# Optimization experiments

Hardware: AMD Instinct MI355X
Metric: run time of the kernel (lower is better)

## Reference

```python
import jax, jax.numpy as jnp
import numpy as np

N_LEVELS = 16
N_FEAT = 2
LOG2_HASHMAP = 19
HASHMAP_SIZE = 1 << LOG2_HASHMAP
BASE_RES = 16.0
FINEST_RES = 512.0
B_POINTS = 524288


def ngp_hash(coords, log2_size):
    # instant-NGP spatial hash: xor of coord * prime, masked to table size.
    # uint32 arithmetic wraps exactly like torch int32 for the masked low bits.
    primes = jnp.array([1, 2654435761, 805459861], dtype=jnp.uint32)
    c = coords.astype(jnp.uint32) * primes  # (..., 3)
    h = c[..., 0] ^ c[..., 1] ^ c[..., 2]
    return (h & jnp.uint32((1 << log2_size) - 1)).astype(jnp.int32)


def setup_inputs() -> dict:
    key = jax.random.key(0)
    k1, k2 = jax.random.split(key)
    # points strictly inside the unit bounding box
    x = jax.random.uniform(k1, (B_POINTS, 3), jnp.float32) * 0.998 + 0.001
    # embedding table init U(-1e-4, 1e-4), matching init_debug_vector
    table = (jax.random.uniform(k2, (HASHMAP_SIZE * N_LEVELS, N_FEAT), jnp.float32) * 2.0 - 1.0) * 1e-4
    box_min = jnp.zeros((3,), jnp.float32)
    box_max = jnp.ones((3,), jnp.float32)
    return {"x": x, "table": table, "box_min": box_min, "box_max": box_max}


def reference(x, table, box_min, box_max):
    B = x.shape[0]
    # per-level growth factor b and resolutions (L,1,1)
    b = jnp.exp((jnp.log(FINEST_RES) - jnp.log(BASE_RES)) / (N_LEVELS - 1))
    resolution = jnp.floor(BASE_RES * b ** jnp.arange(N_LEVELS, dtype=jnp.float32))[:, None, None]
    bmin = box_min[None, None]  # (1,1,3)
    bmax = box_max[None, None]
    grid_size = (bmax - bmin) / resolution  # (L,1,3)

    xl = x[None]  # (1,B,3)
    bottom_left = ((xl - bmin) / grid_size).astype(jnp.int32)  # (L,B,3)
    voxel_min = bottom_left.astype(x.dtype) * grid_size + bmin  # (L,B,3)
    voxel_max = voxel_min + grid_size

    # 8 corner offsets, i-major order as in the torch box_offsets
    offsets = jnp.array([[i, j, k] for i in (0, 1) for j in (0, 1) for k in (0, 1)], dtype=jnp.int32)  # (8,3)
    corners = bottom_left[:, :, None, :] + offsets[None, None]  # (L,B,8,3)

    level_off = (jnp.arange(N_LEVELS, dtype=jnp.int32) * HASHMAP_SIZE)[:, None, None]
    idx = ngp_hash(corners, LOG2_HASHMAP) + level_off  # (L,B,8)
    ve = table[idx]  # (L,B,8,F) hash-gather

    w = (xl - voxel_min) / (voxel_max - voxel_min)  # (L,B,3)
    wx, wy, wz = w[..., 0:1], w[..., 1:2], w[..., 2:3]
    c00 = ve[:, :, 0] * (1 - wx) + ve[:, :, 4] * wx
    c01 = ve[:, :, 1] * (1 - wx) + ve[:, :, 5] * wx
    c10 = ve[:, :, 2] * (1 - wx) + ve[:, :, 6] * wx
    c11 = ve[:, :, 3] * (1 - wx) + ve[:, :, 7] * wx
    c0 = c00 * (1 - wy) + c10 * wy
    c1 = c01 * (1 - wy) + c11 * wy
    c = c0 * (1 - wz) + c1 * wz  # (L,B,F)

    # permute(1,2,0) then flatten last two dims -> (B, F*L)
    return jnp.transpose(c, (1, 2, 0)).reshape(B, N_FEAT * N_LEVELS)
```

## Files before the change

kernel.cpp:

```cpp
#include <hip/hip_runtime.h>
#include <cstdint>


constexpr int NLEV = 16;
constexpr uint32_t HM_MASK = (1u << 19) - 1;

__device__ __constant__ double c_res[NLEV] = {
    16.0, 20.0, 25.0, 32.0, 40.0, 50.0, 64.0, 80.0,
    101.0, 128.0, 161.0, 203.0, 256.0, 322.0, 406.0, 512.0
};

__device__ __forceinline__ void ngp_eval_point(
    int b, int lev,
    const float* __restrict__ x,
    const float2* __restrict__ tab2,
    float bm0, float bm1, float bm2,
    float d0, float d1, float d2,
    float& f0, float& f1)
{
    const float fx0 = x[3 * b + 0];
    const float fx1 = x[3 * b + 1];
    const float fx2 = x[3 * b + 2];

    const double res = c_res[lev];
    const double g0 = (double)d0 / res;
    const double g1 = (double)d1 / res;
    const double g2 = (double)d2 / res;
    const double q0 = (double)(fx0 - bm0) / g0;
    const double q1 = (double)(fx1 - bm1) / g1;
    const double q2 = (double)(fx2 - bm2) / g2;
    const int i0 = (int)q0;
    const int i1 = (int)q1;
    const int i2 = (int)q2;
    const float w0 = (float)(q0 - (double)i0);
    const float w1 = (float)(q1 - (double)i1);
    const float w2 = (float)(q2 - (double)i2);

    const uint32_t P1 = 2654435761u, P2 = 805459861u;
    const uint32_t h0a = (uint32_t)i0;
    const uint32_t h0b = h0a + 1u;
    const uint32_t h1a = (uint32_t)i1 * P1;
    const uint32_t h1b = h1a + P1;
    const uint32_t h2a = (uint32_t)i2 * P2;
    const uint32_t h2b = h2a + P2;
    const uint32_t base = (uint32_t)lev << 19;

    const float2 v000 = tab2[base + ((h0a ^ h1a ^ h2a) & HM_MASK)];
    const float2 v001 = tab2[base + ((h0a ^ h1a ^ h2b) & HM_MASK)];
    const float2 v010 = tab2[base + ((h0a ^ h1b ^ h2a) & HM_MASK)];
    const float2 v011 = tab2[base + ((h0a ^ h1b ^ h2b) & HM_MASK)];
    const float2 v100 = tab2[base + ((h0b ^ h1a ^ h2a) & HM_MASK)];
    const float2 v101 = tab2[base + ((h0b ^ h1a ^ h2b) & HM_MASK)];
    const float2 v110 = tab2[base + ((h0b ^ h1b ^ h2a) & HM_MASK)];
    const float2 v111 = tab2[base + ((h0b ^ h1b ^ h2b) & HM_MASK)];

    const float u0 = 1.0f - w0, u1 = 1.0f - w1, u2 = 1.0f - w2;
    const float waa = u1 * u2;
    const float wab = u1 * w2;
    const float wba = w1 * u2;
    const float wbb = w1 * w2;

    f0 = u0 * (waa * v000.x + wab * v001.x + wba * v010.x + wbb * v011.x)
       + w0 * (waa * v100.x + wab * v101.x + wba * v110.x + wbb * v111.x);
    f1 = u0 * (waa * v000.y + wab * v001.y + wba * v010.y + wbb * v011.y)
       + w0 * (waa * v100.y + wab * v101.y + wba * v110.y + wbb * v111.y);
}

__global__ __launch_bounds__(256)
void ngp_levels_kernel(const float* __restrict__ x,
                       const float* __restrict__ table,
                       const float* __restrict__ box_min,
                       const float* __restrict__ box_max,
                       float2* __restrict__ ws,
                       int B, int chunks)
{
    const int xcd = blockIdx.x & 7;
    const int s   = blockIdx.x >> 3;
    const int lev   = (s < chunks) ? xcd : (15 - xcd);
    const int chunk = (s < chunks) ? s : (s - chunks);
    const int b = chunk * 256 + threadIdx.x;
    if (b >= B) return;

    const float bm0 = box_min[0], bm1 = box_min[1], bm2 = box_min[2];
    const float d0 = box_max[0] - bm0;
    const float d1 = box_max[1] - bm1;
    const float d2 = box_max[2] - bm2;

    float f0, f1;
    ngp_eval_point(b, lev, x, (const float2*)table,
                   bm0, bm1, bm2, d0, d1, d2, f0, f1);

    ws[(size_t)chunk * (NLEV * 256) + lev * 256 + threadIdx.x]
        = make_float2(f0, f1);
}

constexpr int LDS_STRIDE = 257;

__global__ __launch_bounds__(256)
void ngp_transpose_kernel(const float2* __restrict__ ws,
                          float* __restrict__ out,
                          int B)
{
    __shared__ float lds[32 * LDS_STRIDE];

    const int t  = threadIdx.x;
    const int c  = blockIdx.x;
    const int P0 = c * 256;

    const float2* __restrict__ wsc = ws + (size_t)c * (NLEV * 256);
#pragma unroll
    for (int l = 0; l < NLEV; ++l) {
        const float2 v = wsc[l * 256 + t];
        lds[(2 * l)     * LDS_STRIDE + t] = v.x;
        lds[(2 * l + 1) * LDS_STRIDE + t] = v.y;
    }
    __syncthreads();

    const int p_lo = t >> 3;
    const int f    = (t >> 2) & 1;
    const int l0   = (t & 3) * 4;
#pragma unroll
    for (int j = 0; j < 8; ++j) {
        const int p = j * 32 + p_lo;
        float4 v;
        v.x = lds[(2 * (l0 + 0) + f) * LDS_STRIDE + p];
        v.y = lds[(2 * (l0 + 1) + f) * LDS_STRIDE + p];
        v.z = lds[(2 * (l0 + 2) + f) * LDS_STRIDE + p];
        v.w = lds[(2 * (l0 + 3) + f) * LDS_STRIDE + p];
        *(float4*)(out + (size_t)P0 * 32 + j * 1024 + t * 4) = v;
    }
}

__global__ __launch_bounds__(256)
void ngp_embed_fused_kernel(const float* __restrict__ x,
                            const float* __restrict__ table,
                            const float* __restrict__ box_min,
                            const float* __restrict__ box_max,
                            float* __restrict__ out,
                            int B)
{
    const int gid = blockIdx.x * 256 + threadIdx.x;
    const int b = gid >> 4;
    const int l = gid & 15;
    if (b >= B) return;

    const float bm0 = box_min[0], bm1 = box_min[1], bm2 = box_min[2];
    const float d0 = box_max[0] - bm0;
    const float d1 = box_max[1] - bm1;
    const float d2 = box_max[2] - bm2;

    float f0, f1;
    ngp_eval_point(b, l, x, (const float2*)table,
                   bm0, bm1, bm2, d0, d1, d2, f0, f1);

    out[b * 32 + l]      = f0;
    out[b * 32 + 16 + l] = f1;
}

extern "C" void kernel_launch(void* const* d_in, const int* in_sizes, int n_in,
                              void* d_out, int out_size, void* d_ws, size_t ws_size,
                              hipStream_t stream) {
    const float* x       = (const float*)d_in[0];
    const float* table   = (const float*)d_in[1];
    const float* box_min = (const float*)d_in[2];
    const float* box_max = (const float*)d_in[3];
    float* out = (float*)d_out;

    const int B = in_sizes[0] / 3;
    const size_t ws_needed = (size_t)B * NLEV * sizeof(float2);

    if (ws_size >= ws_needed && (B % 256) == 0) {
        const int chunks = B / 256;
        const int gridA = 8 * 2 * chunks;
        hipLaunchKernelGGL(ngp_levels_kernel, dim3(gridA), dim3(256), 0, stream,
                           x, table, box_min, box_max, (float2*)d_ws, B, chunks);
        const int gridB = B / 256;
        hipLaunchKernelGGL(ngp_transpose_kernel, dim3(gridB), dim3(256), 0, stream,
                           (const float2*)d_ws, out, B);
    } else {
        const int total = B * NLEV;
        const int blocks = (total + 255) / 256;
        hipLaunchKernelGGL(ngp_embed_fused_kernel, dim3(blocks), dim3(256), 0, stream,
                           x, table, box_min, box_max, out, B);
    }
}
```

Before: 341.4 us.

## Fuse level evaluation and transpose via per-chunk last-block counter

Merges the per-level evaluation kernel and the transpose kernel into one launch. Each block writes its level result to the workspace with agent-scope atomic stores and bumps a per-chunk counter, and the sixteenth block to finish a chunk reads all levels back and writes the transposed output through LDS in two halves. A small kernel zeroes the counters first. The aim is to remove the second pass's launch and scheduling gap and let the transpose overlap with the gathers, at the cost of atomics, a tail of serial work in the last blocks, and a memory-ordering scheme that relies on relaxed atomics plus a compiler barrier.

```diff
diff --git a/kernel.cpp b/kernel.cpp
--- a/kernel.cpp
+++ b/kernel.cpp
@@ -67,6 +67,98 @@
 }
 
 __global__ __launch_bounds__(256)
+void ngp_zero_counters(int* __restrict__ counters, int n)
+{
+    const int i = blockIdx.x * 256 + threadIdx.x;
+    if (i < n) counters[i] = 0;
+}
+
+__global__ __launch_bounds__(256)
+void ngp_fused_tail_kernel(const float* __restrict__ x,
+                           const float* __restrict__ table,
+                           const float* __restrict__ box_min,
+                           const float* __restrict__ box_max,
+                           float2* __restrict__ ws,
+                           int* __restrict__ counters,
+                           float* __restrict__ out,
+                           int B, int chunks)
+{
+    __shared__ float lds[32 * 129];
+    __shared__ int s_last;
+
+    const int xcd = blockIdx.x & 7;
+    const int s   = blockIdx.x >> 3;
+    const int lev   = (s < chunks) ? xcd : (15 - xcd);
+    const int chunk = (s < chunks) ? s : (s - chunks);
+    const int t = threadIdx.x;
+    const int b = chunk * 256 + t;
+
+    const float bm0 = box_min[0], bm1 = box_min[1], bm2 = box_min[2];
+    const float d0 = box_max[0] - bm0;
+    const float d1 = box_max[1] - bm1;
+    const float d2 = box_max[2] - bm2;
+
+    float f0, f1;
+    ngp_eval_point(b, lev, x, (const float2*)table,
+                   bm0, bm1, bm2, d0, d1, d2, f0, f1);
+
+    {
+        float2 v = make_float2(f0, f1);
+        unsigned long long raw;
+        __builtin_memcpy(&raw, &v, 8);
+        __hip_atomic_store(
+            (unsigned long long*)&ws[(size_t)chunk * (NLEV * 256) + lev * 256 + t],
+            raw, __ATOMIC_RELAXED, __HIP_MEMORY_SCOPE_AGENT);
+    }
+
+    __syncthreads();
+
+    if (t == 0) {
+        const int old = atomicAdd(&counters[chunk], 1);
+        s_last = (old == NLEV - 1);
+    }
+    __syncthreads();
+    if (!s_last) return;
+
+    asm volatile("" ::: "memory");
+
+    const float2* __restrict__ wsc = ws + (size_t)chunk * (NLEV * 256);
+    const int p_lo = t >> 3;
+    const int f    = (t >> 2) & 1;
+    const int l0   = (t & 3) * 4;
+
+#pragma unroll
+    for (int h = 0; h < 2; ++h) {
+#pragma unroll
+        for (int i = 0; i < 8; ++i) {
+            const int l = 2 * i + (t >> 7);
+            const int p = t & 127;
+            unsigned long long raw = __hip_atomic_load(
+                (const unsigned long long*)&wsc[l * 256 + h * 128 + p],
+                __ATOMIC_RELAXED, __HIP_MEMORY_SCOPE_AGENT);
+            float2 v;
+            __builtin_memcpy(&v, &raw, 8);
+            lds[(2 * l)     * 129 + p] = v.x;
+            lds[(2 * l + 1) * 129 + p] = v.y;
+        }
+        __syncthreads();
+
+        float* outh = out + ((size_t)chunk * 256 + h * 128) * 32;
+#pragma unroll
+        for (int j = 0; j < 4; ++j) {
+            const int p = j * 32 + p_lo;
+            float4 o;
+            o.x = lds[(2 * (l0 + 0) + f) * 129 + p];
+            o.y = lds[(2 * (l0 + 1) + f) * 129 + p];
+            o.z = lds[(2 * (l0 + 2) + f) * 129 + p];
+            o.w = lds[(2 * (l0 + 3) + f) * 129 + p];
+            *(float4*)(outh + j * 1024 + t * 4) = o;
+        }
+        __syncthreads();
+    }
+}
+
+__global__ __launch_bounds__(256)
 void ngp_levels_kernel(const float* __restrict__ x,
                        const float* __restrict__ table,
                        const float* __restrict__ box_min,
@@ -167,15 +259,24 @@
     float* out = (float*)d_out;
 
     const int B = in_sizes[0] / 3;
-    const size_t ws_needed = (size_t)B * NLEV * sizeof(float2);
-
-    if (ws_size >= ws_needed && (B % 256) == 0) {
-        const int chunks = B / 256;
+    const int chunks = B / 256;
+    const size_t ws_data  = (size_t)B * NLEV * sizeof(float2);
+    const size_t ws_fused = ws_data + (size_t)chunks * sizeof(int);
+
+    if ((B % 256) == 0 && ws_size >= ws_fused) {
+        int* counters = (int*)((char*)d_ws + ws_data);
+        const int zblocks = (chunks + 255) / 256;
+        hipLaunchKernelGGL(ngp_zero_counters, dim3(zblocks), dim3(256), 0, stream,
+                           counters, chunks);
+        const int gridA = 8 * 2 * chunks;
+        hipLaunchKernelGGL(ngp_fused_tail_kernel, dim3(gridA), dim3(256), 0, stream,
+                           x, table, box_min, box_max,
+                           (float2*)d_ws, counters, out, B, chunks);
+    } else if ((B % 256) == 0 && ws_size >= ws_data) {
         const int gridA = 8 * 2 * chunks;
         hipLaunchKernelGGL(ngp_levels_kernel, dim3(gridA), dim3(256), 0, stream,
                            x, table, box_min, box_max, (float2*)d_ws, B, chunks);
-        const int gridB = B / 256;
-        hipLaunchKernelGGL(ngp_transpose_kernel, dim3(gridB), dim3(256), 0, stream,
+        hipLaunchKernelGGL(ngp_transpose_kernel, dim3(chunks), dim3(256), 0, stream,
                            (const float2*)d_ws, out, B);
     } else {
         const int total = B * NLEV;
```

Result: slower. 451.6 us (+32.3%).
